# Kernel tuning notes

Hardware: AMD Instinct MI355X
Metric: run time of the kernel (lower is better)

## Reference

```python
import jax, jax.numpy as jnp
import numpy as np

B, T, C = 4, 1024, 1024  # batch, tokens, channel (== head `size`)
H = 8                    # num_heads


def setup_inputs() -> dict:
    key = jax.random.key(0)
    kd, kq, kk, kv = jax.random.split(key, 4)
    data = jax.random.normal(kd, (B, T, C), dtype=jnp.float32)
    # torch nn.Linear(size,size,bias=False) weight is [out,in]; one per head, stacked on axis 0
    s = 1.0 / np.sqrt(C)
    Wq = jax.random.uniform(kq, (H, C, C), dtype=jnp.float32, minval=-s, maxval=s)
    Wk = jax.random.uniform(kk, (H, C, C), dtype=jnp.float32, minval=-s, maxval=s)
    Wv = jax.random.uniform(kv, (H, C, C), dtype=jnp.float32, minval=-s, maxval=s)
    return {"data": data, "Wq": Wq, "Wk": Wk, "Wv": Wv}


def reference(data, Wq, Wk, Wv):
    # per-head projections: y = x @ W.T  -> [B,H,T,C]
    q = jnp.einsum('btc,hdc->bhtd', data, Wq)
    k = jnp.einsum('btc,hdc->bhtd', data, Wk)
    v = jnp.einsum('btc,hdc->bhtd', data, Wv)
    scale = 1.0 / jnp.sqrt(jnp.asarray(C, dtype=data.dtype))
    scores = jnp.einsum('bhtd,bhsd->bhts', q, k) * scale  # [B,H,T,T]
    causal = jnp.tril(jnp.ones((T, T), dtype=bool))
    scores = jnp.where(causal, scores, -jnp.inf)
    w = jax.nn.softmax(scores, axis=-1)
    out = jnp.einsum('bhts,bhsd->bhtd', w, v)            # [B,H,T,C]
    # torch.cat over heads on last dim == [B,T,H,C] reshape to [B,T,H*C]
    return out.transpose(0, 2, 1, 3).reshape(B, T, H * C)
```

## Files before the change

kernel.cpp:

```cpp
#include <hip/hip_runtime.h>
#include <hip/hip_fp16.h>


typedef unsigned short u16;
typedef _Float16 f16x8 __attribute__((ext_vector_type(8)));
typedef float f32x4 __attribute__((ext_vector_type(4)));

__device__ __forceinline__ u16 f2h(float f) {
    union { __half h; u16 u; } cv;
    cv.h = __float2half(f);
    return cv.u;
}
__device__ __forceinline__ float h2f(u16 u) {
    union { __half h; u16 u; } cv;
    cv.u = u;
    return __half2float(cv.h);
}

__device__ __forceinline__ void gload_lds16(const u16* g, const u16* lds_base, unsigned off_bytes) {
    unsigned a32 = (unsigned)(uintptr_t)((const char*)lds_base + off_bytes);
    a32 = __builtin_amdgcn_readfirstlane(a32);
    __builtin_amdgcn_global_load_lds(
        (const __attribute__((address_space(1))) void*)(uintptr_t)g,
        (__attribute__((address_space(3))) void*)a32,
        16, 0, 0);
}

#define M_A 0
#define M_B 1
#define M_C 2
#define M_PV 3

template <int MODE>
__global__ __launch_bounds__(512, 2) void mega(
    const u16* __restrict__ dataH, const u16* __restrict__ WvH,
    const u16* __restrict__ WqT, const u16* __restrict__ WkT,
    u16* __restrict__ MTp, u16* __restrict__ Qp, u16* __restrict__ VTa,
    u16* __restrict__ S16, const u16* __restrict__ P16,
    float* __restrict__ outF)
{
    const int C = 1024, T = 1024, HC = 8192;
    const int nb = (MODE == M_A ? 192 : MODE == M_B ? 512 :
                    MODE == M_C ? 768 : 256);
    const int chunk = nb >> 3;
    const int phys = blockIdx.x;
    const int o = (phys & 7) * chunk + (phys >> 3);

    __shared__ u16 lds[8 * 8192];

    const int t = threadIdx.x, w = t >> 6, l = t & 63;
    const int wm = w >> 2, wn = w & 3;
    const int frow = l & 15, fch = l >> 4;
    const int clin = w * 64 + l;
    const int srow = clin >> 2;
    const int sch = (clin & 3) ^ ((clin >> 3) & 3);

    const int NPASS = (MODE == M_PV) ? 2 : 1;

    for (int pass = 0; pass < NPASS; ++pass) {
        const u16 *Ab, *Bb;
        int lda, ldb, ldc, NT, tile_m, tile_n;
        float scale = 1.0f;
        u16* out16 = nullptr;
        float* out32 = nullptr;

        int vfill = -1;
        if (MODE == M_A && o >= 128) vfill = o - 128;
        if (MODE == M_C && o >= 320) vfill = o - 320 + 64;

        if (vfill >= 0) {
            const int vz = vfill >> 4, rem = vfill & 15;
            tile_n = rem & 3; tile_m = rem >> 2;
            Ab = WvH + (size_t)(vz & 7) * C * C + (size_t)tile_m * 256 * C;
            Bb = dataH + (size_t)(vz >> 3) * T * C + (size_t)tile_n * 256 * C;
            lda = C; ldb = C; ldc = T;
            out16 = VTa + (size_t)vz * C * T;
            NT = 16;
        } else if (MODE == M_A) {
            const int h = o >> 4, r = o & 15;
            tile_m = r >> 2; tile_n = r & 3;
            Ab = WkT + (size_t)h * C * C + (size_t)tile_m * 256 * C;
            Bb = WqT + (size_t)h * C * C + (size_t)tile_n * 256 * C;
            lda = C; ldb = C; ldc = C;
            out16 = MTp + (size_t)h * C * C;
            NT = 16;
        } else if (MODE == M_B) {
            const int s = o >> 6, ww = o & 63;
            tile_n = (s & 3) * 8 + (ww & 7);
            tile_m = (s >> 2) * 8 + (ww >> 3);
            Ab = dataH + (size_t)tile_m * 256 * C;
            Bb = MTp + (size_t)(tile_n >> 2) * C * C + (size_t)(tile_n & 3) * 256 * C;
            lda = C; ldb = C; ldc = HC;
            out16 = Qp;
            NT = 16;
        } else if (MODE == M_C) {
            const int qz = o / 10, j = o - qz * 10;
            tile_m = (j >= 1) + (j >= 3) + (j >= 6);
            tile_n = j - (tile_m == 0 ? 0 : tile_m == 1 ? 1 : tile_m == 2 ? 3 : 6);
            Ab = Qp + (size_t)(qz >> 3) * T * HC + (size_t)(qz & 7) * C
                    + (size_t)tile_m * 256 * HC;
            Bb = dataH + (size_t)(qz >> 3) * T * C + (size_t)tile_n * 256 * C;
            lda = HC; ldb = C; ldc = T;
            out16 = S16 + (size_t)qz * T * T;
            scale = 1.0f / 32.0f;
            NT = 16;
        } else {
            const int pz = o >> 3, j = o & 7, x = j & 3, hi = j >> 2;
            tile_m = (pass == 0) ? (hi ? 2 : 3) : (hi ? 1 : 0);
            tile_n = x;
            Ab = P16 + (size_t)pz * T * T + (size_t)tile_m * 256 * T;
            Bb = VTa + (size_t)pz * C * T + (size_t)tile_n * 256 * T;
            lda = T; ldb = T; ldc = HC;
            out32 = outF + (size_t)(pz >> 3) * T * HC + (size_t)(pz & 7) * C;
            NT = (tile_m + 1) * 4;
        }

        const long eA = (long)srow * lda + sch * 8;
        const long eB = (long)srow * ldb + sch * 8;

        f32x4 acc[8][4] = {};
        f16x8 af[4], bf[4];

#define STAGE(DB, MAT, KS, TT) do {                                            \
        const u16* g_ = (MAT == 0 ? Ab + (size_t)(TT) * 64 + (KS) * 32 + eA    \
                                  : Bb + (size_t)(TT) * 64 + (KS) * 32 + eB);  \
        const u16* hb_ = lds + ((((DB) << 2) | ((MAT) << 1) | (KS)) << 13);    \
        gload_lds16(g_, hb_, (unsigned)(w * 64 * 16));                         \
        gload_lds16(g_ + (size_t)128 * (MAT == 0 ? lda : ldb), hb_,            \
                    (unsigned)((512 + w * 64) * 16));                          \
    } while (0)

#define RD(DB, MAT, KS, ROW)                                                   \
    (*(const f16x8*)((const char*)(lds + ((((DB) << 2) | ((MAT) << 1) | (KS)) << 13)) + \
                     ((unsigned)((ROW) * 64 + fch * 16) ^ ((((ROW) >> 1) & 3) << 4))))

#define VM6 do { asm volatile("s_waitcnt vmcnt(6)"); \
                 __builtin_amdgcn_sched_barrier(0); } while (0)
#define VM0 do { asm volatile("s_waitcnt vmcnt(0)"); \
                 __builtin_amdgcn_sched_barrier(0); } while (0)
#define NOPW ((void)0)

#define PH(DB, KS, MH, WAITC, ...) do {                                        \
        if ((MH) == 0) {                                                       \
            _Pragma("unroll") for (int ni = 0; ni < 4; ++ni)                   \
                bf[ni] = RD(DB, 1, KS, wn * 64 + ni * 16 + frow);              \
        }                                                                      \
        _Pragma("unroll") for (int m4 = 0; m4 < 4; ++m4)                       \
            af[m4] = RD(DB, 0, KS, wm * 128 + ((MH) * 4 + m4) * 16 + frow);    \
        __VA_ARGS__;                                                           \
        __builtin_amdgcn_sched_barrier(0);                                     \
        __builtin_amdgcn_s_barrier();                                          \
        asm volatile("s_waitcnt lgkmcnt(0)");                                  \
        __builtin_amdgcn_sched_barrier(0);                                     \
        __builtin_amdgcn_s_setprio(1);                                         \
        _Pragma("unroll") for (int m4 = 0; m4 < 4; ++m4)                       \
            _Pragma("unroll") for (int ni = 0; ni < 4; ++ni)                   \
                acc[(MH) * 4 + m4][ni] = __builtin_amdgcn_mfma_f32_16x16x32_f16( \
                    af[m4], bf[ni], acc[(MH) * 4 + m4][ni], 0, 0, 0);          \
        __builtin_amdgcn_s_setprio(0);                                         \
        __builtin_amdgcn_sched_barrier(0);                                     \
        WAITC;                                                                 \
        __builtin_amdgcn_s_barrier();                                          \
    } while (0)

        STAGE(0, 1, 0, 0); STAGE(0, 0, 0, 0); STAGE(0, 1, 1, 0); STAGE(0, 0, 1, 0);
        STAGE(1, 1, 0, 1); STAGE(1, 0, 0, 1); STAGE(1, 1, 1, 1);
        VM6;
        __builtin_amdgcn_s_barrier();

        for (int tt = 0; tt < NT; tt += 2) {
            const bool more = (tt + 2) < NT;
            PH(0, 0, 0, NOPW, STAGE(1, 0, 1, tt + 1));
            PH(0, 0, 1, NOPW, if (more) STAGE(0, 1, 0, tt + 2));
            PH(0, 1, 0, NOPW, if (more) STAGE(0, 0, 0, tt + 2));
            PH(0, 1, 1, if (more) VM6; else VM0,
                        if (more) STAGE(0, 1, 1, tt + 2));
            PH(1, 0, 0, NOPW, if (more) STAGE(0, 0, 1, tt + 2));
            PH(1, 0, 1, NOPW, if (more) STAGE(1, 1, 0, tt + 3));
            PH(1, 1, 0, NOPW, if (more) STAGE(1, 0, 0, tt + 3));
            PH(1, 1, 1, if (more) VM6; else VM0,
                        if (more) STAGE(1, 1, 1, tt + 3));
        }
#undef PH
#undef RD
#undef STAGE
#undef VM6
#undef VM0
#undef NOPW

        const int r0 = (l >> 4) * 4, cc = l & 15;
#pragma unroll
        for (int mi = 0; mi < 8; ++mi) {
#pragma unroll
            for (int r = 0; r < 4; ++r) {
                size_t grow = (size_t)(tile_m * 256 + wm * 128 + mi * 16 + r0 + r);
#pragma unroll
                for (int ni = 0; ni < 4; ++ni) {
                    int gcol = tile_n * 256 + wn * 64 + ni * 16 + cc;
                    float v = acc[mi][ni][r] * scale;
                    if (MODE == M_PV)
                        out32[grow * ldc + gcol] = v;
                    else
                        out16[grow * ldc + gcol] = f2h(v);
                }
            }
        }
    }
}

__global__ __launch_bounds__(256) void softmax16(
    const u16* __restrict__ S, u16* __restrict__ P)
{
    const int T = 1024;
    const int tq = blockIdx.x, z = blockIdx.y;
    const u16* row = S + ((size_t)z * T + tq) * T;
    u16* prow = P + ((size_t)z * T + tq) * T;
    const int n = tq + 1, tid = threadIdx.x, i0 = tid * 4;
    const int nw = ((tq >> 8) + 1) << 8;

    ushort4 v = ((const ushort4*)row)[tid];
    float e0 = (i0 + 0 < n) ? h2f(v.x) : -1e30f;
    float e1 = (i0 + 1 < n) ? h2f(v.y) : -1e30f;
    float e2 = (i0 + 2 < n) ? h2f(v.z) : -1e30f;
    float e3 = (i0 + 3 < n) ? h2f(v.w) : -1e30f;

    float m = fmaxf(fmaxf(e0, e1), fmaxf(e2, e3));
#pragma unroll
    for (int o = 1; o < 64; o <<= 1) m = fmaxf(m, __shfl_xor(m, o));
    __shared__ float red[4];
    if ((tid & 63) == 0) red[tid >> 6] = m;
    __syncthreads();
    m = fmaxf(fmaxf(red[0], red[1]), fmaxf(red[2], red[3]));

    float p0 = __expf(e0 - m), p1 = __expf(e1 - m);
    float p2 = __expf(e2 - m), p3 = __expf(e3 - m);
    float s = p0 + p1 + p2 + p3;
#pragma unroll
    for (int o = 1; o < 64; o <<= 1) s += __shfl_xor(s, o);
    __shared__ float red2[4];
    if ((tid & 63) == 0) red2[tid >> 6] = s;
    __syncthreads();
    const float inv = 1.0f / (red2[0] + red2[1] + red2[2] + red2[3]);

    if (i0 < nw) {
        ushort4 o4;
        o4.x = f2h(p0 * inv); o4.y = f2h(p1 * inv);
        o4.z = f2h(p2 * inv); o4.w = f2h(p3 * inv);
        ((ushort4*)prow)[tid] = o4;
    }
}

__global__ __launch_bounds__(256) void cast_setup(
    const float* __restrict__ data, const float* __restrict__ Wq,
    const float* __restrict__ Wk, const float* __restrict__ Wv,
    u16* __restrict__ dataH, u16* __restrict__ WqT,
    u16* __restrict__ WkT, u16* __restrict__ WvH)
{
    const int z = blockIdx.z, tx = threadIdx.x, ty = threadIdx.y;
    if (z < 16) {
        const int h = z & 7;
        const float* src = ((z >> 3) ? Wk : Wq) + (size_t)h * 1048576;
        u16* dst = ((z >> 3) ? WkT : WqT) + (size_t)h * 1048576;
        const int r0 = blockIdx.y * 32, c0 = blockIdx.x * 32;
        __shared__ float tile[32][33];
        for (int i = ty; i < 32; i += 8)
            tile[i][tx] = src[(size_t)(r0 + i) * 1024 + c0 + tx];
        __syncthreads();
        for (int i = ty; i < 32; i += 8)
            dst[(size_t)(c0 + i) * 1024 + r0 + tx] = f2h(tile[tx][i]);
    } else {
        const int tid = ty * 32 + tx;
        const int bid = blockIdx.y * 32 + blockIdx.x;
        const int reps = (z == 16) ? 4 : 8;
        const float* src = (z == 16) ? data : Wv;
        u16* dst = (z == 16) ? dataH : WvH;
        for (int k2 = 0; k2 < reps; ++k2) {
            int i = (k2 * 1024 + bid) * 256 + tid;
            float4 v = ((const float4*)src)[i];
            ushort4 o4;
            o4.x = f2h(v.x); o4.y = f2h(v.y); o4.z = f2h(v.z); o4.w = f2h(v.w);
            ((ushort4*)dst)[i] = o4;
        }
    }
}

extern "C" void kernel_launch(void* const* d_in, const int* in_sizes, int n_in,
                              void* d_out, int out_size, void* d_ws, size_t ws_size,
                              hipStream_t stream)
{
    (void)in_sizes; (void)n_in; (void)out_size; (void)ws_size;
    const int B = 4, T = 1024, C = 1024, H = 8;
    const int BT = B * T, HC = H * C;

    const float* data = (const float*)d_in[0];
    const float* Wq = (const float*)d_in[1];
    const float* Wk = (const float*)d_in[2];
    const float* Wv = (const float*)d_in[3];
    float* out = (float*)d_out;

    char* p = (char*)d_ws;
    const size_t nData = (size_t)BT * C;
    const size_t nW = (size_t)H * C * C;
    const size_t nAll = (size_t)BT * HC;
    const size_t nS = (size_t)B * H * T * T;
    u16* dataH = (u16*)p; p += nData * 2;
    u16* WvH = (u16*)p; p += nW * 2;
    u16* WqT = (u16*)p; p += nW * 2;
    u16* WkT = (u16*)p; p += nW * 2;
    u16* MTp = (u16*)p; p += nW * 2;
    u16* Qp = (u16*)p; p += nAll * 2;
    u16* VTa = (u16*)p; p += nAll * 2;
    u16* S16 = (u16*)p; p += nS * 2;
    u16* P16 = (u16*)p; p += nS * 2;

    cast_setup<<<dim3(32, 32, 18), dim3(32, 8), 0, stream>>>(
        data, Wq, Wk, Wv, dataH, WqT, WkT, WvH);

    mega<M_A><<<dim3(192), dim3(512), 0, stream>>>(
        dataH, WvH, WqT, WkT, MTp, Qp, VTa, S16, P16, out);

    mega<M_B><<<dim3(512), dim3(512), 0, stream>>>(
        dataH, WvH, WqT, WkT, MTp, Qp, VTa, S16, P16, out);

    mega<M_C><<<dim3(768), dim3(512), 0, stream>>>(
        dataH, WvH, WqT, WkT, MTp, Qp, VTa, S16, P16, out);

    softmax16<<<dim3(T, B * H), dim3(256), 0, stream>>>(S16, P16);

    mega<M_PV><<<dim3(256), dim3(512), 0, stream>>>(
        dataH, WvH, WqT, WkT, MTp, Qp, VTa, S16, P16, out);
}
```

Measured before the change: 364.6 us.

## Fuse causal softmax into the PV GEMM kernel and drop the softmax launch

New measurement: 450.5 us. 1.24x slower.

```diff
diff --git a/kernel.cpp b/kernel.cpp
--- a/kernel.cpp
+++ b/kernel.cpp
@@ -36,7 +36,7 @@
     const u16* __restrict__ dataH, const u16* __restrict__ WvH,
     const u16* __restrict__ WqT, const u16* __restrict__ WkT,
     u16* __restrict__ MTp, u16* __restrict__ Qp, u16* __restrict__ VTa,
-    u16* __restrict__ S16, const u16* __restrict__ P16,
+    u16* __restrict__ S16, u16* __restrict__ P16,
     float* __restrict__ outF)
 {
     const int C = 1024, T = 1024, HC = 8192;
@@ -115,6 +115,58 @@
             NT = (tile_m + 1) * 4;
         }
 
+        if (MODE == M_PV) {
+            const int pz = o >> 3;
+            const int Kend = NT * 64;
+            const u16* Sb = S16 + (size_t)pz * T * T + (size_t)tile_m * 256 * T;
+            u16* Pb = P16 + (size_t)pz * T * T + (size_t)tile_m * 256 * T;
+            for (int rr = w; rr < 256; rr += 8) {
+                const int nrow = tile_m * 256 + rr + 1;
+                const u16* rp = Sb + (size_t)rr * T;
+                float ev[16];
+#pragma unroll
+                for (int j = 0; j < 4; ++j) {
+                    const int col = j * 256 + l * 4;
+                    if (col < Kend) {
+                        ushort4 v4 = *(const ushort4*)(rp + col);
+                        ev[j * 4 + 0] = (col + 0 < nrow) ? h2f(v4.x) : -3.0e38f;
+                        ev[j * 4 + 1] = (col + 1 < nrow) ? h2f(v4.y) : -3.0e38f;
+                        ev[j * 4 + 2] = (col + 2 < nrow) ? h2f(v4.z) : -3.0e38f;
+                        ev[j * 4 + 3] = (col + 3 < nrow) ? h2f(v4.w) : -3.0e38f;
+                    } else {
+                        ev[j * 4 + 0] = -3.0e38f; ev[j * 4 + 1] = -3.0e38f;
+                        ev[j * 4 + 2] = -3.0e38f; ev[j * 4 + 3] = -3.0e38f;
+                    }
+                }
+                float mx = -3.0e38f;
+#pragma unroll
+                for (int e = 0; e < 16; ++e) mx = fmaxf(mx, ev[e]);
+#pragma unroll
+                for (int od = 1; od < 64; od <<= 1) mx = fmaxf(mx, __shfl_xor(mx, od));
+                float sum = 0.f;
+#pragma unroll
+                for (int e = 0; e < 16; ++e) { ev[e] = __expf(ev[e] - mx); sum += ev[e]; }
+#pragma unroll
+                for (int od = 1; od < 64; od <<= 1) sum += __shfl_xor(sum, od);
+                const float inv = 1.0f / sum;
+#pragma unroll
+                for (int j = 0; j < 4; ++j) {
+                    const int col = j * 256 + l * 4;
+                    if (col < Kend) {
+                        ushort4 o4;
+                        o4.x = f2h(ev[j * 4 + 0] * inv);
+                        o4.y = f2h(ev[j * 4 + 1] * inv);
+                        o4.z = f2h(ev[j * 4 + 2] * inv);
+                        o4.w = f2h(ev[j * 4 + 3] * inv);
+                        *(ushort4*)(Pb + (size_t)rr * T + col) = o4;
+                    }
+                }
+            }
+            asm volatile("s_waitcnt vmcnt(0)");
+            __builtin_amdgcn_sched_barrier(0);
+            __builtin_amdgcn_s_barrier();
+        }
+
         const long eA = (long)srow * lda + sch * 8;
         const long eB = (long)srow * ldb + sch * 8;
 
@@ -205,48 +257,6 @@
                 }
             }
         }
-    }
-}
-
-__global__ __launch_bounds__(256) void softmax16(
-    const u16* __restrict__ S, u16* __restrict__ P)
-{
-    const int T = 1024;
-    const int tq = blockIdx.x, z = blockIdx.y;
-    const u16* row = S + ((size_t)z * T + tq) * T;
-    u16* prow = P + ((size_t)z * T + tq) * T;
-    const int n = tq + 1, tid = threadIdx.x, i0 = tid * 4;
-    const int nw = ((tq >> 8) + 1) << 8;
-
-    ushort4 v = ((const ushort4*)row)[tid];
-    float e0 = (i0 + 0 < n) ? h2f(v.x) : -1e30f;
-    float e1 = (i0 + 1 < n) ? h2f(v.y) : -1e30f;
-    float e2 = (i0 + 2 < n) ? h2f(v.z) : -1e30f;
-    float e3 = (i0 + 3 < n) ? h2f(v.w) : -1e30f;
-
-    float m = fmaxf(fmaxf(e0, e1), fmaxf(e2, e3));
-#pragma unroll
-    for (int o = 1; o < 64; o <<= 1) m = fmaxf(m, __shfl_xor(m, o));
-    __shared__ float red[4];
-    if ((tid & 63) == 0) red[tid >> 6] = m;
-    __syncthreads();
-    m = fmaxf(fmaxf(red[0], red[1]), fmaxf(red[2], red[3]));
-
-    float p0 = __expf(e0 - m), p1 = __expf(e1 - m);
-    float p2 = __expf(e2 - m), p3 = __expf(e3 - m);
-    float s = p0 + p1 + p2 + p3;
-#pragma unroll
-    for (int o = 1; o < 64; o <<= 1) s += __shfl_xor(s, o);
-    __shared__ float red2[4];
-    if ((tid & 63) == 0) red2[tid >> 6] = s;
-    __syncthreads();
-    const float inv = 1.0f / (red2[0] + red2[1] + red2[2] + red2[3]);
-
-    if (i0 < nw) {
-        ushort4 o4;
-        o4.x = f2h(p0 * inv); o4.y = f2h(p1 * inv);
-        o4.z = f2h(p2 * inv); o4.w = f2h(p3 * inv);
-        ((ushort4*)prow)[tid] = o4;
     }
 }
 
@@ -325,8 +335,6 @@
     mega<M_C><<<dim3(768), dim3(512), 0, stream>>>(
         dataH, WvH, WqT, WkT, MTp, Qp, VTa, S16, P16, out);
 
-    softmax16<<<dim3(T, B * H), dim3(256), 0, stream>>>(S16, P16);
-
     mega<M_PV><<<dim3(256), dim3(512), 0, stream>>>(
         dataH, WvH, WqT, WkT, MTp, Qp, VTa, S16, P16, out);
 }
```
